# Performance work log

Measured on AMD Instinct MI355X. Metric: run time of the kernel, lower is better.

The kernel has to match this reference:

```python
import jax, jax.numpy as jnp
import numpy as np

MAX_SEQ_LEN = 2048
ADJ_SCALE = 0.1


def setup_inputs() -> dict:
    key = jax.random.key(0)
    k1, k2, k3 = jax.random.split(key, 3)
    B, L, H, D = 8, 2048, 16, 64
    x = jax.random.normal(k1, (B, L, H, D), dtype=jnp.float32)
    W = jax.random.normal(k2, (D, D), dtype=jnp.float32) * (1.0 / np.sqrt(D))
    b = jax.random.normal(k3, (D,), dtype=jnp.float32) * 0.02
    gate = jnp.ones((1,), dtype=jnp.float32) * 0.5  # betweenness_gate init
    return {"x": x, "W": W, "b": b, "gate": gate}


def reference(x, W, b, gate):
    B, L, H, D = x.shape
    # --- RoPE frequency table (precompute_freqs_cis) ---
    base_freqs = 1.0 / (10000.0 ** (jnp.arange(0, D, 2, dtype=jnp.float32) / D))  # (D/2,)
    t = jnp.arange(L, dtype=jnp.float32)
    freqs = t[:, None] * base_freqs[None, :]          # (L, D/2)
    fcos, fsin = jnp.cos(freqs), jnp.sin(freqs)

    # --- betweenness: only consecutive-pair distances are ever used ---
    content = jnp.einsum('blhd,ed->blhe', x, W) + b    # nn.Linear(dim, dim)
    d1 = jnp.linalg.norm(content[:, 1:] - content[:, :-1], axis=-1)   # (B, L-1, H)  d(i, i+1)
    d2 = jnp.linalg.norm(content[:, 2:] - content[:, :-2], axis=-1)   # (B, L-2, H)  d(i, i+2)
    direct = d2
    path = d1[:, :-1] + d1[:, 1:]
    score = jax.nn.relu(1.0 - (path - direct) / jnp.maximum(direct, 1e-6))  # (B, L-2, H)
    betweenness = jnp.zeros((B, L, H), x.dtype).at[:, 1:L - 1].set(score / (L - 2))

    # --- betweenness-adjusted interpolated RoPE (vectorized over positions) ---
    adjust = gate[0] * (betweenness - 0.5) * ADJ_SCALE               # (B, L, H)
    pos = jnp.arange(L, dtype=jnp.float32)[None, :, None]
    adj_pos = jnp.clip(pos + adjust, 0.0, MAX_SEQ_LEN - 1)
    lo = jnp.floor(adj_pos).astype(jnp.int32)
    hi = jnp.ceil(adj_pos).astype(jnp.int32)
    frac = (adj_pos - lo)[..., None]                                 # (B, L, H, 1)
    cos_i = (1.0 - frac) * fcos[lo] + frac * fcos[hi]                # (B, L, H, D/2)
    sin_i = (1.0 - frac) * fsin[lo] + frac * fsin[hi]

    x_even = x[..., 0::2]
    x_odd = x[..., 1::2]
    out_even = x_even * cos_i - x_odd * sin_i
    out_odd = x_odd * cos_i + x_even * sin_i
    out = jnp.stack([out_even, out_odd], axis=-1).reshape(B, L, H, D)  # re-interleave
    return out
```

## Files before the change

### kernel.cpp

```cpp
#include <hip/hip_runtime.h>

#define L_SEQ 2048
#define HEADS 16
#define DIM   64
#define TILE  64
#define XROWS 66
#define XPITCH 68
#define DROWS 80

typedef __attribute__((ext_vector_type(8))) short bf16x8;
typedef __attribute__((ext_vector_type(4))) float f32x4;

static __device__ __forceinline__ unsigned short f2bf_rtne(float f) {
    unsigned int u = __builtin_bit_cast(unsigned int, f);
    u += 0x7fffu + ((u >> 16) & 1u);
    return (unsigned short)(u >> 16);
}
static __device__ __forceinline__ unsigned int pk2(float a, float b) {
    return __builtin_amdgcn_perm(__builtin_bit_cast(unsigned int, b),
                                 __builtin_bit_cast(unsigned int, a), 0x07060302u);
}
static __device__ __forceinline__ unsigned short f2bf_trunc(float f) {
    return (unsigned short)(__builtin_bit_cast(unsigned int, f) >> 16);
}

#define SWZ(row, col) ((row) * 64 + ((col) ^ (((row) & 7) * 8)))

__global__ void prep_w_kernel(const float* __restrict__ W, unsigned short* __restrict__ wbf) {
    int i = blockIdx.x * 256 + threadIdx.x;
    if (i < DIM * DIM) wbf[i] = f2bf_rtne(W[i]);
}

static __device__ __forceinline__ bf16x8 load_bfrag(const unsigned short* wbf,
                                                    const float* W, int n, int k0) {
    if (wbf) return *(const bf16x8*)(wbf + n * 64 + k0);
    const float* wr = W + n * 64 + k0;
    float4 w0 = *(const float4*)wr;
    float4 w1 = *(const float4*)(wr + 4);
    uint4 p;
    p.x = pk2(w0.x, w0.y); p.y = pk2(w0.z, w0.w);
    p.z = pk2(w1.x, w1.y); p.w = pk2(w1.z, w1.w);
    return __builtin_bit_cast(bf16x8, p);
}

__global__ __launch_bounds__(512) void betweenness_rope_kernel(
    const float* __restrict__ x, const float* __restrict__ W,
    const unsigned short* __restrict__ wbf, const float* __restrict__ gate,
    float* __restrict__ out)
{
    __shared__ float xs[XROWS * XPITCH];
    __shared__ unsigned short dl[DROWS * 64];
    __shared__ unsigned short el[DROWS * 64];
    __shared__ float n1s[65];
    __shared__ float g1s[64];
    __shared__ float2 fl[TILE];

    const int tid  = threadIdx.x;
    const int lane = tid & 63;
    const int wave = tid >> 6;
    const int la   = lane & 15, lg = lane >> 4;
    const int l0   = blockIdx.x * TILE;
    const int h    = blockIdx.y;
    const int b    = blockIdx.z;
    const int bh_off = (b * L_SEQ * HEADS + h) * DIM;

    for (int c = tid; c < XROWS * 16; c += 512) {
        int r = c >> 4, q = c & 15;
        int g = l0 - 1 + r; g = max(0, min(L_SEQ - 1, g));
        float4 v = *(const float4*)(x + bh_off + g * (HEADS * DIM) + q * 4);
        *(float4*)&xs[r * XPITCH + q * 4] = v;
    }
    __syncthreads();

    for (int c = tid; c < DROWS * 8; c += 512) {
        int r = c >> 3, c0 = (c & 7) * 8;
        uint4 o = {0u, 0u, 0u, 0u};
        if (r <= 64) {
            float4 a0 = *(float4*)&xs[r * XPITCH + c0];
            float4 a1 = *(float4*)&xs[r * XPITCH + c0 + 4];
            float4 b0 = *(float4*)&xs[(r + 1) * XPITCH + c0];
            float4 b1 = *(float4*)&xs[(r + 1) * XPITCH + c0 + 4];
            o.x = pk2(b0.x - a0.x, b0.y - a0.y);
            o.y = pk2(b0.z - a0.z, b0.w - a0.w);
            o.z = pk2(b1.x - a1.x, b1.y - a1.y);
            o.w = pk2(b1.z - a1.z, b1.w - a1.w);
        }
        *(uint4*)&dl[SWZ(r, c0)] = o;
    }
    __syncthreads();

    for (int job = wave; job < 20; job += 8) {
        int mt = job >> 2, nt = job & 3;
        bf16x8 a0 = *(const bf16x8*)&dl[SWZ(16 * mt + la, lg * 8)];
        bf16x8 a1 = *(const bf16x8*)&dl[SWZ(16 * mt + la, lg * 8 + 32)];
        bf16x8 b0 = load_bfrag(wbf, W, 16 * nt + la, lg * 8);
        bf16x8 b1 = load_bfrag(wbf, W, 16 * nt + la, lg * 8 + 32);
        f32x4 acc = {0.f, 0.f, 0.f, 0.f};
        acc = __builtin_amdgcn_mfma_f32_16x16x32_bf16(a0, b0, acc, 0, 0, 0);
        acc = __builtin_amdgcn_mfma_f32_16x16x32_bf16(a1, b1, acc, 0, 0, 0);
        #pragma unroll
        for (int q = 0; q < 4; ++q)
            el[SWZ(16 * mt + lg * 4 + q, 16 * nt + la)] = f2bf_trunc(acc[q]);
    }
    __syncthreads();

    for (int job = wave; job < 9; job += 8) {
        int mt = (job < 5) ? job : job - 5;
        int nt = (job < 5) ? job : job - 4;
        f32x4 g = {0.f, 0.f, 0.f, 0.f};
        #pragma unroll
        for (int kt = 0; kt < 2; ++kt) {
            int cb = lg * 8 + kt * 32;
            bf16x8 a  = *(const bf16x8*)&el[SWZ(16 * mt + la, cb)];
            bf16x8 bb = *(const bf16x8*)&el[SWZ(16 * nt + la, cb)];
            g = __builtin_amdgcn_mfma_f32_16x16x32_bf16(a, bb, g, 0, 0, 0);
        }
        #pragma unroll
        for (int q = 0; q < 4; ++q) {
            int R = 16 * mt + lg * 4 + q, C = 16 * nt + la;
            if (C == R && R < 65) n1s[R] = g[q];
            if (C == R + 1 && R < 64) g1s[R] = g[q];
        }
    }
    __syncthreads();

    if (tid < TILE) {
        const float gate0 = gate[0];
        int r = tid, l = l0 + r;
        float a1 = n1s[r], b1 = n1s[r + 1], gg = g1s[r];
        float d1a = sqrtf(a1), d1b = sqrtf(b1);
        float dd  = sqrtf(fmaxf(a1 + b1 + 2.f * gg, 0.f));
        float sc  = fmaxf(1.f - ((d1a + d1b) - dd) / fmaxf(dd, 1e-6f), 0.f);
        float bet = (l >= 1 && l <= L_SEQ - 2) ? sc * (1.f / (L_SEQ - 2)) : 0.f;
        float adjust = gate0 * (bet - 0.5f) * 0.1f;
        float ap  = fminf(fmaxf((float)l + adjust, 0.f), (float)(L_SEQ - 1));
        float flo = floorf(ap);
        fl[r] = make_float2(flo, ap - flo);
    }
    __syncthreads();

    {
        const int j = lane & 31, half = lane >> 5;
        const float fjr = __builtin_exp2f(-0.4152410118609203f * (float)j)
                        * 0.15915494309189535f;
        const float cf = __builtin_amdgcn_cosf(fjr);
        const float sf = __builtin_amdgcn_sinf(fjr);
        const float cfm1 = cf - 1.0f;
        const int r0w = wave * 2 + half;
        const float* xbase = &xs[(r0w + 1) * XPITCH + 2 * j];
        float* obase = out + bh_off + (l0 + r0w) * (HEADS * DIM) + 2 * j;
        #pragma unroll
        for (int it = 0; it < 4; ++it) {
            int r = it * 16 + r0w;
            float2 ff = fl[r];
            float t0 = ff.x * fjr;
            float rv = t0 - floorf(t0);
            float c_lo = __builtin_amdgcn_cosf(rv);
            float s_lo = __builtin_amdgcn_sinf(rv);
            float u = fmaf(ff.y, cfm1, 1.0f);
            float v = ff.y * sf;
            float ci = fmaf(-s_lo, v, c_lo * u);
            float si = fmaf(c_lo, v, s_lo * u);
            float2 xv = *(const float2*)(xbase + it * 16 * XPITCH);
            float2 o;
            o.x = xv.x * ci - xv.y * si;
            o.y = fmaf(xv.y, ci, xv.x * si);
            *(float2*)(obase + it * 16 * (HEADS * DIM)) = o;
        }
    }
}

extern "C" void kernel_launch(void* const* d_in, const int* in_sizes, int n_in,
                              void* d_out, int out_size, void* d_ws, size_t ws_size,
                              hipStream_t stream) {
    const float* x    = (const float*)d_in[0];
    const float* W    = (const float*)d_in[1];
    const float* gate = (const float*)d_in[3];
    float* out = (float*)d_out;

    const int B = in_sizes[0] / (L_SEQ * HEADS * DIM);

    unsigned short* wbf = nullptr;
    if (ws_size >= (size_t)(DIM * DIM * sizeof(unsigned short))) {
        wbf = (unsigned short*)d_ws;
        prep_w_kernel<<<16, 256, 0, stream>>>(W, wbf);
    }

    dim3 grid(L_SEQ / TILE, HEADS, B);
    betweenness_rope_kernel<<<grid, 512, 0, stream>>>(x, W, wbf, gate, out);
}
```

Baseline: 47.26 us.

## Shrink tile to 32 rows, drop x staging in LDS, vectorize RoPE stores

Halves the sequence tile to 32 rows and uses 128-thread blocks with launch bounds set for 8 blocks per CU. The x tile is no longer staged in shared memory: the difference rows are built straight from global loads, and the RoPE stage re-reads x from global as float4. Each lane now handles two frequency pairs so loads and stores are 16 bytes wide. The aim is higher occupancy and less LDS traffic and synchronisation, at the cost of reading x from global twice, more halo overhead per tile, and wasted MFMA rows on the padded tiles.

```diff
diff --git a/kernel.cpp b/kernel.cpp
--- a/kernel.cpp
+++ b/kernel.cpp
@@ -3,10 +3,8 @@
 #define L_SEQ 2048
 #define HEADS 16
 #define DIM   64
-#define TILE  64
-#define XROWS 66
-#define XPITCH 68
-#define DROWS 80
+#define TILE  32
+#define NROWS 34
 
 typedef __attribute__((ext_vector_type(8))) short bf16x8;
 typedef __attribute__((ext_vector_type(4))) float f32x4;
@@ -43,16 +41,15 @@
     return __builtin_bit_cast(bf16x8, p);
 }
 
-__global__ __launch_bounds__(512) void betweenness_rope_kernel(
+__global__ __launch_bounds__(128, 8) void betweenness_rope_kernel(
     const float* __restrict__ x, const float* __restrict__ W,
     const unsigned short* __restrict__ wbf, const float* __restrict__ gate,
     float* __restrict__ out)
 {
-    __shared__ float xs[XROWS * XPITCH];
-    __shared__ unsigned short dl[DROWS * 64];
-    __shared__ unsigned short el[DROWS * 64];
-    __shared__ float n1s[65];
-    __shared__ float g1s[64];
+    __shared__ unsigned short dl[NROWS * 64];
+    __shared__ unsigned short el[NROWS * 64];
+    __shared__ float n1s[NROWS];
+    __shared__ float g1s[33];
     __shared__ float2 fl[TILE];
 
     const int tid  = threadIdx.x;
@@ -64,62 +61,63 @@
     const int b    = blockIdx.z;
     const int bh_off = (b * L_SEQ * HEADS + h) * DIM;
 
-    for (int c = tid; c < XROWS * 16; c += 512) {
-        int r = c >> 4, q = c & 15;
-        int g = l0 - 1 + r; g = max(0, min(L_SEQ - 1, g));
-        float4 v = *(const float4*)(x + bh_off + g * (HEADS * DIM) + q * 4);
-        *(float4*)&xs[r * XPITCH + q * 4] = v;
-    }
-    __syncthreads();
-
-    for (int c = tid; c < DROWS * 8; c += 512) {
-        int r = c >> 3, c0 = (c & 7) * 8;
-        uint4 o = {0u, 0u, 0u, 0u};
-        if (r <= 64) {
-            float4 a0 = *(float4*)&xs[r * XPITCH + c0];
-            float4 a1 = *(float4*)&xs[r * XPITCH + c0 + 4];
-            float4 b0 = *(float4*)&xs[(r + 1) * XPITCH + c0];
-            float4 b1 = *(float4*)&xs[(r + 1) * XPITCH + c0 + 4];
+    #pragma unroll
+    for (int k = 0; k < 3; ++k) {
+        int s = tid + k * 128;
+        if (s < NROWS * 8) {
+            int r = s >> 3, c0 = (s & 7) * 8;
+            int g0 = max(0, min(L_SEQ - 1, l0 - 1 + r));
+            int g1 = max(0, min(L_SEQ - 1, l0 + r));
+            const float* p0 = x + bh_off + g0 * (HEADS * DIM) + c0;
+            const float* p1 = x + bh_off + g1 * (HEADS * DIM) + c0;
+            float4 a0 = *(const float4*)p0, a1 = *(const float4*)(p0 + 4);
+            float4 b0 = *(const float4*)p1, b1 = *(const float4*)(p1 + 4);
+            uint4 o;
             o.x = pk2(b0.x - a0.x, b0.y - a0.y);
             o.y = pk2(b0.z - a0.z, b0.w - a0.w);
             o.z = pk2(b1.x - a1.x, b1.y - a1.y);
             o.w = pk2(b1.z - a1.z, b1.w - a1.w);
+            *(uint4*)&dl[SWZ(r, c0)] = o;
         }
-        *(uint4*)&dl[SWZ(r, c0)] = o;
     }
     __syncthreads();
 
-    for (int job = wave; job < 20; job += 8) {
+    for (int job = wave; job < 12; job += 2) {
         int mt = job >> 2, nt = job & 3;
-        bf16x8 a0 = *(const bf16x8*)&dl[SWZ(16 * mt + la, lg * 8)];
-        bf16x8 a1 = *(const bf16x8*)&dl[SWZ(16 * mt + la, lg * 8 + 32)];
+        int arow = min(16 * mt + la, NROWS - 1);
+        bf16x8 a0 = *(const bf16x8*)&dl[SWZ(arow, lg * 8)];
+        bf16x8 a1 = *(const bf16x8*)&dl[SWZ(arow, lg * 8 + 32)];
         bf16x8 b0 = load_bfrag(wbf, W, 16 * nt + la, lg * 8);
         bf16x8 b1 = load_bfrag(wbf, W, 16 * nt + la, lg * 8 + 32);
         f32x4 acc = {0.f, 0.f, 0.f, 0.f};
         acc = __builtin_amdgcn_mfma_f32_16x16x32_bf16(a0, b0, acc, 0, 0, 0);
         acc = __builtin_amdgcn_mfma_f32_16x16x32_bf16(a1, b1, acc, 0, 0, 0);
         #pragma unroll
-        for (int q = 0; q < 4; ++q)
-            el[SWZ(16 * mt + lg * 4 + q, 16 * nt + la)] = f2bf_trunc(acc[q]);
+        for (int q = 0; q < 4; ++q) {
+            int R = 16 * mt + lg * 4 + q;
+            if (R < NROWS) el[SWZ(R, 16 * nt + la)] = f2bf_trunc(acc[q]);
+        }
     }
     __syncthreads();
 
-    for (int job = wave; job < 9; job += 8) {
-        int mt = (job < 5) ? job : job - 5;
-        int nt = (job < 5) ? job : job - 4;
+    for (int job = wave; job < 5; job += 2) {
+        int mt = (job < 3) ? job : job - 3;
+        int nt = (job < 3) ? job : job - 2;
+        int arow = min(16 * mt + la, NROWS - 1);
+        int brow = min(16 * nt + la, NROWS - 1);
         f32x4 g = {0.f, 0.f, 0.f, 0.f};
         #pragma unroll
         for (int kt = 0; kt < 2; ++kt) {
             int cb = lg * 8 + kt * 32;
-            bf16x8 a  = *(const bf16x8*)&el[SWZ(16 * mt + la, cb)];
-            bf16x8 bb = *(const bf16x8*)&el[SWZ(16 * nt + la, cb)];
+            bf16x8 a  = *(const bf16x8*)&el[SWZ(arow, cb)];
+            bf16x8 bb = *(const bf16x8*)&el[SWZ(brow, cb)];
             g = __builtin_amdgcn_mfma_f32_16x16x32_bf16(a, bb, g, 0, 0, 0);
         }
         #pragma unroll
         for (int q = 0; q < 4; ++q) {
             int R = 16 * mt + lg * 4 + q, C = 16 * nt + la;
-            if (C == R && R < 65) n1s[R] = g[q];
-            if (C == R + 1 && R < 64) g1s[R] = g[q];
+            if (C == R && R < NROWS) n1s[R] = g[q];
+            if (C == R + 1 && R < 33) g1s[R] = g[q];
         }
     }
     __syncthreads();
@@ -140,32 +138,42 @@
     __syncthreads();
 
     {
-        const int j = lane & 31, half = lane >> 5;
-        const float fjr = __builtin_exp2f(-0.4152410118609203f * (float)j)
+        const int j2 = lane & 15;
+        const int rg = lane >> 4;
+        const float fja = __builtin_exp2f(-0.4152410118609203f * (float)(2 * j2))
                         * 0.15915494309189535f;
-        const float cf = __builtin_amdgcn_cosf(fjr);
-        const float sf = __builtin_amdgcn_sinf(fjr);
-        const float cfm1 = cf - 1.0f;
-        const int r0w = wave * 2 + half;
-        const float* xbase = &xs[(r0w + 1) * XPITCH + 2 * j];
-        float* obase = out + bh_off + (l0 + r0w) * (HEADS * DIM) + 2 * j;
+        const float fjb = __builtin_exp2f(-0.4152410118609203f * (float)(2 * j2 + 1))
+                        * 0.15915494309189535f;
+        const float cfa = __builtin_amdgcn_cosf(fja), sfa = __builtin_amdgcn_sinf(fja);
+        const float cfb = __builtin_amdgcn_cosf(fjb), sfb = __builtin_amdgcn_sinf(fjb);
+        const float cfma = cfa - 1.0f, cfmb = cfb - 1.0f;
         #pragma unroll
         for (int it = 0; it < 4; ++it) {
-            int r = it * 16 + r0w;
+            int r = it * 8 + wave * 4 + rg;
+            int l = l0 + r;
             float2 ff = fl[r];
-            float t0 = ff.x * fjr;
-            float rv = t0 - floorf(t0);
-            float c_lo = __builtin_amdgcn_cosf(rv);
-            float s_lo = __builtin_amdgcn_sinf(rv);
-            float u = fmaf(ff.y, cfm1, 1.0f);
-            float v = ff.y * sf;
-            float ci = fmaf(-s_lo, v, c_lo * u);
-            float si = fmaf(c_lo, v, s_lo * u);
-            float2 xv = *(const float2*)(xbase + it * 16 * XPITCH);
-            float2 o;
-            o.x = xv.x * ci - xv.y * si;
-            o.y = fmaf(xv.y, ci, xv.x * si);
-            *(float2*)(obase + it * 16 * (HEADS * DIM)) = o;
+            const float* xp = x + bh_off + l * (HEADS * DIM) + 4 * j2;
+            float4 xv = *(const float4*)xp;
+            float ta = ff.x * fja;
+            float rva = ta - floorf(ta);
+            float cla = __builtin_amdgcn_cosf(rva), sla = __builtin_amdgcn_sinf(rva);
+            float ua = fmaf(ff.y, cfma, 1.0f);
+            float va = ff.y * sfa;
+            float cia = fmaf(-sla, va, cla * ua);
+            float sia = fmaf(cla, va, sla * ua);
+            float tb = ff.x * fjb;
+            float rvb = tb - floorf(tb);
+            float clb = __builtin_amdgcn_cosf(rvb), slb = __builtin_amdgcn_sinf(rvb);
+            float ub = fmaf(ff.y, cfmb, 1.0f);
+            float vb = ff.y * sfb;
+            float cib = fmaf(-slb, vb, clb * ub);
+            float sib = fmaf(clb, vb, slb * ub);
+            float4 o;
+            o.x = xv.x * cia - xv.y * sia;
+            o.y = fmaf(xv.y, cia, xv.x * sia);
+            o.z = xv.z * cib - xv.w * sib;
+            o.w = fmaf(xv.w, cib, xv.z * sib);
+            *(float4*)(out + bh_off + l * (HEADS * DIM) + 4 * j2) = o;
         }
     }
 }
@@ -187,5 +195,5 @@
     }
 
     dim3 grid(L_SEQ / TILE, HEADS, B);
-    betweenness_rope_kernel<<<grid, 512, 0, stream>>>(x, W, wbf, gate, out);
+    betweenness_rope_kernel<<<grid, 128, 0, stream>>>(x, W, wbf, gate, out);
 }
```

Result: slower. 57.66 us (+22.0%).

## Compute row norms and adjacent dot products directly from MFMA registers

Applied to the files above, without the earlier changes.

Replaces the two-stage approach (store projected differences to LDS in bf16, then a second MFMA Gram-matrix pass for the diagonals) with a direct computation. Squared norms and adjacent-row dot products are taken from the MFMA accumulators in fp32 and reduced with cross-lane shuffles, with partial sums per column block combined across four waves. It also halves the tile to 32 rows with 256-thread blocks, which doubles the block count and the halo overhead per row. This removes one LDS round trip, one barrier and the bf16 truncation of the projection, at the cost of more shuffle work.

```diff
diff --git a/kernel.cpp b/kernel.cpp
--- a/kernel.cpp
+++ b/kernel.cpp
@@ -3,10 +3,10 @@
 #define L_SEQ 2048
 #define HEADS 16
 #define DIM   64
-#define TILE  64
-#define XROWS 66
+#define TILE  32
+#define XROWS 34
 #define XPITCH 68
-#define DROWS 80
+#define DROWS 48
 
 typedef __attribute__((ext_vector_type(8))) short bf16x8;
 typedef __attribute__((ext_vector_type(4))) float f32x4;
@@ -19,9 +19,6 @@
 static __device__ __forceinline__ unsigned int pk2(float a, float b) {
     return __builtin_amdgcn_perm(__builtin_bit_cast(unsigned int, b),
                                  __builtin_bit_cast(unsigned int, a), 0x07060302u);
-}
-static __device__ __forceinline__ unsigned short f2bf_trunc(float f) {
-    return (unsigned short)(__builtin_bit_cast(unsigned int, f) >> 16);
 }
 
 #define SWZ(row, col) ((row) * 64 + ((col) ^ (((row) & 7) * 8)))
@@ -43,39 +40,38 @@
     return __builtin_bit_cast(bf16x8, p);
 }
 
-__global__ __launch_bounds__(512) void betweenness_rope_kernel(
+__global__ __launch_bounds__(256) void betweenness_rope_kernel(
     const float* __restrict__ x, const float* __restrict__ W,
     const unsigned short* __restrict__ wbf, const float* __restrict__ gate,
     float* __restrict__ out)
 {
     __shared__ float xs[XROWS * XPITCH];
     __shared__ unsigned short dl[DROWS * 64];
-    __shared__ unsigned short el[DROWS * 64];
-    __shared__ float n1s[65];
-    __shared__ float g1s[64];
+    __shared__ float psq[4][36];
+    __shared__ float ppr[4][36];
     __shared__ float2 fl[TILE];
 
     const int tid  = threadIdx.x;
     const int lane = tid & 63;
-    const int wave = tid >> 6;
+    const int wv   = tid >> 6;
     const int la   = lane & 15, lg = lane >> 4;
     const int l0   = blockIdx.x * TILE;
     const int h    = blockIdx.y;
     const int b    = blockIdx.z;
     const int bh_off = (b * L_SEQ * HEADS + h) * DIM;
 
-    for (int c = tid; c < XROWS * 16; c += 512) {
+    for (int c = tid; c < XROWS * 16; c += 256) {
         int r = c >> 4, q = c & 15;
-        int g = l0 - 1 + r; g = max(0, min(L_SEQ - 1, g));
-        float4 v = *(const float4*)(x + bh_off + g * (HEADS * DIM) + q * 4);
-        *(float4*)&xs[r * XPITCH + q * 4] = v;
-    }
-    __syncthreads();
-
-    for (int c = tid; c < DROWS * 8; c += 512) {
-        int r = c >> 3, c0 = (c & 7) * 8;
+        int g = max(0, min(L_SEQ - 1, l0 - 1 + r));
+        *(float4*)&xs[r * XPITCH + q * 4] =
+            *(const float4*)(x + bh_off + g * (HEADS * DIM) + q * 4);
+    }
+    __syncthreads();
+
+    for (int r = tid >> 3; r < DROWS; r += 32) {
+        int c0 = (tid & 7) * 8;
         uint4 o = {0u, 0u, 0u, 0u};
-        if (r <= 64) {
+        if (r <= 32) {
             float4 a0 = *(float4*)&xs[r * XPITCH + c0];
             float4 a1 = *(float4*)&xs[r * XPITCH + c0 + 4];
             float4 b0 = *(float4*)&xs[(r + 1) * XPITCH + c0];
@@ -89,37 +85,60 @@
     }
     __syncthreads();
 
-    for (int job = wave; job < 20; job += 8) {
-        int mt = job >> 2, nt = job & 3;
-        bf16x8 a0 = *(const bf16x8*)&dl[SWZ(16 * mt + la, lg * 8)];
-        bf16x8 a1 = *(const bf16x8*)&dl[SWZ(16 * mt + la, lg * 8 + 32)];
-        bf16x8 b0 = load_bfrag(wbf, W, 16 * nt + la, lg * 8);
-        bf16x8 b1 = load_bfrag(wbf, W, 16 * nt + la, lg * 8 + 32);
-        f32x4 acc = {0.f, 0.f, 0.f, 0.f};
-        acc = __builtin_amdgcn_mfma_f32_16x16x32_bf16(a0, b0, acc, 0, 0, 0);
-        acc = __builtin_amdgcn_mfma_f32_16x16x32_bf16(a1, b1, acc, 0, 0, 0);
-        #pragma unroll
-        for (int q = 0; q < 4; ++q)
-            el[SWZ(16 * mt + lg * 4 + q, 16 * nt + la)] = f2bf_trunc(acc[q]);
-    }
-    __syncthreads();
-
-    for (int job = wave; job < 9; job += 8) {
-        int mt = (job < 5) ? job : job - 5;
-        int nt = (job < 5) ? job : job - 4;
-        f32x4 g = {0.f, 0.f, 0.f, 0.f};
-        #pragma unroll
-        for (int kt = 0; kt < 2; ++kt) {
-            int cb = lg * 8 + kt * 32;
-            bf16x8 a  = *(const bf16x8*)&el[SWZ(16 * mt + la, cb)];
-            bf16x8 bb = *(const bf16x8*)&el[SWZ(16 * nt + la, cb)];
-            g = __builtin_amdgcn_mfma_f32_16x16x32_bf16(a, bb, g, 0, 0, 0);
-        }
-        #pragma unroll
-        for (int q = 0; q < 4; ++q) {
-            int R = 16 * mt + lg * 4 + q, C = 16 * nt + la;
-            if (C == R && R < 65) n1s[R] = g[q];
-            if (C == R + 1 && R < 64) g1s[R] = g[q];
+    {
+        bf16x8 b0 = load_bfrag(wbf, W, 16 * wv + la, lg * 8);
+        bf16x8 b1 = load_bfrag(wbf, W, 16 * wv + la, lg * 8 + 32);
+        f32x4 e0 = {0.f,0.f,0.f,0.f}, e1 = {0.f,0.f,0.f,0.f}, e2 = {0.f,0.f,0.f,0.f};
+        {
+            bf16x8 aA0 = *(const bf16x8*)&dl[SWZ(la,      lg * 8)];
+            bf16x8 aA1 = *(const bf16x8*)&dl[SWZ(la,      lg * 8 + 32)];
+            bf16x8 aB0 = *(const bf16x8*)&dl[SWZ(16 + la, lg * 8)];
+            bf16x8 aB1 = *(const bf16x8*)&dl[SWZ(16 + la, lg * 8 + 32)];
+            bf16x8 aC0 = *(const bf16x8*)&dl[SWZ(32 + la, lg * 8)];
+            bf16x8 aC1 = *(const bf16x8*)&dl[SWZ(32 + la, lg * 8 + 32)];
+            e0 = __builtin_amdgcn_mfma_f32_16x16x32_bf16(aA0, b0, e0, 0, 0, 0);
+            e0 = __builtin_amdgcn_mfma_f32_16x16x32_bf16(aA1, b1, e0, 0, 0, 0);
+            e1 = __builtin_amdgcn_mfma_f32_16x16x32_bf16(aB0, b0, e1, 0, 0, 0);
+            e1 = __builtin_amdgcn_mfma_f32_16x16x32_bf16(aB1, b1, e1, 0, 0, 0);
+            e2 = __builtin_amdgcn_mfma_f32_16x16x32_bf16(aC0, b0, e2, 0, 0, 0);
+            e2 = __builtin_amdgcn_mfma_f32_16x16x32_bf16(aC1, b1, e2, 0, 0, 0);
+        }
+        float upA = __shfl(e0[0], (lane + 16) & 63);
+        float upB = __shfl(e1[0], (lane + 16) & 63);
+        float upC = __shfl(e2[0], (lane + 16) & 63);
+        float sq0[4], sq1[4], pr0[4], pr1[4], sq2;
+        #pragma unroll
+        for (int q = 0; q < 4; ++q) { sq0[q] = e0[q] * e0[q]; sq1[q] = e1[q] * e1[q]; }
+        sq2 = e2[0] * e2[0];
+        #pragma unroll
+        for (int q = 0; q < 3; ++q) { pr0[q] = e0[q] * e0[q + 1]; pr1[q] = e1[q] * e1[q + 1]; }
+        pr0[3] = e0[3] * ((lg == 3) ? upB : upA);
+        pr1[3] = e1[3] * ((lg == 3) ? upC : upB);
+        #pragma unroll
+        for (int m = 1; m < 16; m <<= 1) {
+            #pragma unroll
+            for (int q = 0; q < 4; ++q) {
+                sq0[q] += __shfl_xor(sq0[q], m, 64);
+                sq1[q] += __shfl_xor(sq1[q], m, 64);
+                pr0[q] += __shfl_xor(pr0[q], m, 64);
+                pr1[q] += __shfl_xor(pr1[q], m, 64);
+            }
+            sq2 += __shfl_xor(sq2, m, 64);
+        }
+        if (la == 0) {
+            #pragma unroll
+            for (int q = 0; q < 4; ++q) {
+                psq[wv][4 * lg + q] = sq0[q];
+                ppr[wv][4 * lg + q] = pr0[q];
+            }
+        } else if (la == 1) {
+            #pragma unroll
+            for (int q = 0; q < 4; ++q) {
+                psq[wv][16 + 4 * lg + q] = sq1[q];
+                ppr[wv][16 + 4 * lg + q] = pr1[q];
+            }
+        } else if (la == 2 && lg == 0) {
+            psq[wv][32] = sq2;
         }
     }
     __syncthreads();
@@ -127,9 +146,11 @@
     if (tid < TILE) {
         const float gate0 = gate[0];
         int r = tid, l = l0 + r;
-        float a1 = n1s[r], b1 = n1s[r + 1], gg = g1s[r];
-        float d1a = sqrtf(a1), d1b = sqrtf(b1);
-        float dd  = sqrtf(fmaxf(a1 + b1 + 2.f * gg, 0.f));
+        float n1a = psq[0][r]     + psq[1][r]     + psq[2][r]     + psq[3][r];
+        float n1b = psq[0][r + 1] + psq[1][r + 1] + psq[2][r + 1] + psq[3][r + 1];
+        float gg  = ppr[0][r]     + ppr[1][r]     + ppr[2][r]     + ppr[3][r];
+        float d1a = sqrtf(n1a), d1b = sqrtf(n1b);
+        float dd  = sqrtf(fmaxf(n1a + n1b + 2.f * gg, 0.f));
         float sc  = fmaxf(1.f - ((d1a + d1b) - dd) / fmaxf(dd, 1e-6f), 0.f);
         float bet = (l >= 1 && l <= L_SEQ - 2) ? sc * (1.f / (L_SEQ - 2)) : 0.f;
         float adjust = gate0 * (bet - 0.5f) * 0.1f;
@@ -146,12 +167,12 @@
         const float cf = __builtin_amdgcn_cosf(fjr);
         const float sf = __builtin_amdgcn_sinf(fjr);
         const float cfm1 = cf - 1.0f;
-        const int r0w = wave * 2 + half;
+        const int r0w = wv * 2 + half;
         const float* xbase = &xs[(r0w + 1) * XPITCH + 2 * j];
         float* obase = out + bh_off + (l0 + r0w) * (HEADS * DIM) + 2 * j;
         #pragma unroll
         for (int it = 0; it < 4; ++it) {
-            int r = it * 16 + r0w;
+            int r = it * 8 + r0w;
             float2 ff = fl[r];
             float t0 = ff.x * fjr;
             float rv = t0 - floorf(t0);
@@ -161,11 +182,11 @@
             float v = ff.y * sf;
             float ci = fmaf(-s_lo, v, c_lo * u);
             float si = fmaf(c_lo, v, s_lo * u);
-            float2 xv = *(const float2*)(xbase + it * 16 * XPITCH);
+            float2 xv = *(const float2*)(xbase + it * 8 * XPITCH);
             float2 o;
             o.x = xv.x * ci - xv.y * si;
             o.y = fmaf(xv.y, ci, xv.x * si);
-            *(float2*)(obase + it * 16 * (HEADS * DIM)) = o;
+            *(float2*)(obase + it * 8 * (HEADS * DIM)) = o;
         }
     }
 }
@@ -187,5 +208,5 @@
     }
 
     dim3 grid(L_SEQ / TILE, HEADS, B);
-    betweenness_rope_kernel<<<grid, 512, 0, stream>>>(x, W, wbf, gate, out);
-}
+    betweenness_rope_kernel<<<grid, 256, 0, stream>>>(x, W, wbf, gate, out);
+}
```

Measured after the change: 50.15 us. 1.06x slower.
